# Kernel optimization log

Hardware: AMD Instinct MI355X
Metric: run time of the kernel (lower is better)

Reference implementation:

```python
import jax, jax.numpy as jnp
from jax import lax
import numpy as np

KSIZE = 3  # dynamic depthwise kernel size
DN = ('NCHW', 'OIHW', 'NCHW')


def setup_inputs() -> dict:
    key = jax.random.key(0)
    ks = jax.random.split(key, 6)
    B, C, H, W = 16, 64, 192, 192
    x = jax.random.normal(ks[0], (B, C, H, W), dtype=jnp.float32)
    k_v = jax.random.normal(ks[1], (B, 64), dtype=jnp.float32)
    # kernel-generating MLP (torch nn.Linear weights, y = x @ W.T), scaled for stability
    W1 = jax.random.normal(ks[2], (64, 64), dtype=jnp.float32) * (1.0 / np.sqrt(64))
    W2 = jax.random.normal(ks[3], (C * KSIZE * KSIZE, 64), dtype=jnp.float32) * (1.0 / np.sqrt(64))
    # static Conv2d(C, C, 3, padding=1)
    conv_w = jax.random.normal(ks[4], (C, C, 3, 3), dtype=jnp.float32) * (1.0 / np.sqrt(C * 9))
    conv_b = jax.random.normal(ks[5], (C,), dtype=jnp.float32) * 0.01
    return {"x": x, "k_v": k_v, "W1": W1, "W2": W2, "conv_w": conv_w, "conv_b": conv_b}


def reference(x, k_v, W1, W2, conv_w, conv_b):
    b, c, h, w = x.shape
    pad = (KSIZE - 1) // 2
    # kernel = Linear -> LeakyReLU(0.1) -> Linear, viewed as (b*c, 1, k, k)
    hid = jax.nn.leaky_relu(k_v @ W1.T, negative_slope=0.1)            # (b, 64)
    kern = (hid @ W2.T).reshape(b * c, 1, KSIZE, KSIZE)                # (b*c, 1, k, k)
    # grouped depthwise conv: one distinct kxk kernel per (batch, channel)
    out = lax.conv_general_dilated(
        x.reshape(1, b * c, h, w), kern,
        window_strides=(1, 1), padding=[(pad, pad), (pad, pad)],
        feature_group_count=b * c, dimension_numbers=DN)
    out = jax.nn.leaky_relu(out, negative_slope=0.1).reshape(b, c, h, w)
    # static 3x3 conv residual branch
    res = lax.conv_general_dilated(
        x, conv_w, window_strides=(1, 1), padding=[(1, 1), (1, 1)],
        dimension_numbers=DN) + conv_b[None, :, None, None]
    return out + res
```

## Files before the change

kernel.cpp:

```cpp
#include <hip/hip_runtime.h>

#define B_ 16
#define C_ 64
#define H_ 192
#define W_ 192
#define TR 4
#define TC 64

typedef short bf16x8 __attribute__((ext_vector_type(8)));
typedef float f32x4  __attribute__((ext_vector_type(4)));

static __device__ __forceinline__ unsigned short f2bf(float f) {
    union { float f; unsigned u; } v; v.f = f;
    unsigned r = v.u + 0x7fff + ((v.u >> 16) & 1);
    return (unsigned short)(r >> 16);
}
static __device__ __forceinline__ float bf2f(unsigned short u) {
    union { unsigned u; float f; } v; v.u = ((unsigned)u) << 16; return v.f;
}
static __device__ __forceinline__ int xsw(int p, int ch) {
    return p * 64 + (((ch >> 3) ^ (p & 7)) << 3) + (ch & 7);
}

__global__ void prep(const float* __restrict__ k_v, const float* __restrict__ W1,
                     const float* __restrict__ W2, const float* __restrict__ conv_w,
                     float* __restrict__ kern, unsigned short* __restrict__ wT) {
    const int blk = blockIdx.x, tid = threadIdx.x;
    if (blk < 16) {
        __shared__ float kv[64], hid[64];
        const int b = blk;
        if (tid < 64) kv[tid] = k_v[b * 64 + tid];
        __syncthreads();
        if (tid < 64) {
            const float4* w4 = (const float4*)(W1 + tid * 64);
            float s = 0.f;
#pragma unroll
            for (int k4 = 0; k4 < 16; ++k4) {
                float4 f = w4[k4];
                s += kv[k4 * 4 + 0] * f.x + kv[k4 * 4 + 1] * f.y
                   + kv[k4 * 4 + 2] * f.z + kv[k4 * 4 + 3] * f.w;
            }
            hid[tid] = s > 0.f ? s : 0.1f * s;
        }
        __syncthreads();
        for (int o = tid; o < 576; o += 256) {
            const float4* w4 = (const float4*)(W2 + o * 64);
            float t = 0.f;
#pragma unroll
            for (int k4 = 0; k4 < 16; ++k4) {
                float4 f = w4[k4];
                t += hid[k4 * 4 + 0] * f.x + hid[k4 * 4 + 1] * f.y
                   + hid[k4 * 4 + 2] * f.z + hid[k4 * 4 + 3] * f.w;
            }
            kern[b * 576 + o] = t;
        }
    } else {
        int idx = (blk - 16) * 256 + tid;
        int tap = idx >> 12;
        int rem = idx & 4095;
        int n = rem >> 6, k = rem & 63;
        wT[idx] = f2bf(conv_w[(n * 64 + k) * 9 + tap]);
    }
}

__global__ __launch_bounds__(256)
void fused_conv(const float* __restrict__ x, const unsigned short* __restrict__ wT,
                const float* __restrict__ kern, const float* __restrict__ conv_b,
                float* __restrict__ out) {
    const int L = blockIdx.x + 3 * (blockIdx.y + 48 * blockIdx.z);
    const int g = L & 7;
    const int s = L >> 3;
    const int bx = s % 3;
    const int sl = s / 3;
    const int by = sl % 48;
    const int b  = (g << 1) + (sl / 48);

    const int tid  = threadIdx.x;
    const int lane = tid & 63;
    const int wv   = tid >> 6;
    const int n0   = lane & 15;
    const int q    = lane >> 4;
    const int r0 = by * TR;
    const int c0 = bx * TC;

    __shared__ __align__(16) unsigned short xs[6 * 66 * 64];

    const unsigned short* wbase = wT + n0 * 64 + q * 8;

    for (int u = tid; u < 768; u += 256) {
        int chg  = u / 96;
        int rest = u - chg * 96;
        int row  = rest >> 4;
        int cg   = rest & 15;
        int gr   = r0 + row - 1;
        bool in  = (gr >= 0 && gr < H_);
        int grc  = in ? gr : 0;
        const float* xp = x + ((size_t)(b * 64 + chg * 8) * H_ + grc) * W_ + c0 + cg * 4;
        float4 f[8];
#pragma unroll
        for (int j = 0; j < 8; ++j)
            f[j] = in ? *(const float4*)(xp + j * H_ * W_) : make_float4(0.f, 0.f, 0.f, 0.f);
#pragma unroll
        for (int e = 0; e < 4; ++e) {
            int p = row * 66 + 1 + cg * 4 + e;
            union { bf16x8 v; unsigned short s8[8]; } pk;
#pragma unroll
            for (int j = 0; j < 8; ++j) pk.s8[j] = f2bf(((const float*)&f[j])[e]);
            *(bf16x8*)(xs + xsw(p, chg * 8)) = pk.v;
        }
    }
    if (tid < 96) {
        int chg  = tid / 12;
        int rest = tid - chg * 12;
        int row  = rest >> 1;
        int sc   = (rest & 1) ? 65 : 0;
        int gr = r0 + row - 1, gc = c0 + sc - 1;
        bool in = (gr >= 0 && gr < H_ && gc >= 0 && gc < W_);
        union { bf16x8 v; unsigned short s8[8]; } pk;
#pragma unroll
        for (int j = 0; j < 8; ++j) {
            float vv = 0.f;
            if (in) vv = x[((size_t)(b * 64 + chg * 8 + j) * H_ + gr) * W_ + gc];
            pk.s8[j] = f2bf(vv);
        }
        *(bf16x8*)(xs + xsw(row * 66 + sc, chg * 8)) = pk.v;
    }

    f32x4 acc[4][4];
#pragma unroll
    for (int i = 0; i < 4; ++i)
#pragma unroll
        for (int j = 0; j < 4; ++j) acc[i][j] = (f32x4){0.f, 0.f, 0.f, 0.f};

    __syncthreads();

    int dr = 0, dc = 0;
#pragma unroll 1
    for (int tap = 0; tap < 9; ++tap) {
        bf16x8 bcur[4][2];
#pragma unroll
        for (int nt = 0; nt < 4; ++nt)
#pragma unroll
            for (int ks = 0; ks < 2; ++ks)
                bcur[nt][ks] = *(const bf16x8*)(wbase + tap * 4096 + nt * 1024 + ks * 32);
#pragma unroll
        for (int cb = 0; cb < 4; ++cb) {
            const int p = (wv + dr) * 66 + cb * 16 + n0 + dc;
            bf16x8 a0 = *(const bf16x8*)(xs + p * 64 + ((q ^ (p & 7)) << 3));
            bf16x8 a1 = *(const bf16x8*)(xs + p * 64 + (((q + 4) ^ (p & 7)) << 3));
#pragma unroll
            for (int nt = 0; nt < 4; ++nt) {
                acc[cb][nt] = __builtin_amdgcn_mfma_f32_16x16x32_bf16(a0, bcur[nt][0], acc[cb][nt], 0, 0, 0);
                acc[cb][nt] = __builtin_amdgcn_mfma_f32_16x16x32_bf16(a1, bcur[nt][1], acc[cb][nt], 0, 0, 0);
            }
        }
        if (++dc == 3) { dc = 0; ++dr; }
    }

    const float* kp = kern + b * 576;
#pragma unroll
    for (int nt = 0; nt < 4; ++nt) {
        const int n = nt * 16 + n0;
        float kw[9];
#pragma unroll
        for (int j = 0; j < 9; ++j) kw[j] = kp[n * 9 + j];
        const float bias = conv_b[n];
        const int gn = n >> 3, n7 = n & 7;
#pragma unroll
        for (int cb = 0; cb < 4; ++cb) {
            const int colb = cb * 16 + q * 4;
            float xw[3][6];
#pragma unroll
            for (int d = 0; d < 3; ++d)
#pragma unroll
                for (int cc = 0; cc < 6; ++cc) {
                    int p = (wv + d) * 66 + colb + cc;
                    xw[d][cc] = bf2f(xs[p * 64 + ((gn ^ (p & 7)) << 3) + n7]);
                }
            float4 st;
#pragma unroll
            for (int r = 0; r < 4; ++r) {
                float dw = 0.f;
#pragma unroll
                for (int d = 0; d < 3; ++d)
#pragma unroll
                    for (int e = 0; e < 3; ++e)
                        dw += kw[d * 3 + e] * xw[d][r + e];
                float v = (dw > 0.f ? dw : 0.1f * dw) + acc[cb][nt][r] + bias;
                ((float*)&st)[r] = v;
            }
            *(float4*)(out + ((size_t)(b * 64 + n) * H_ + (r0 + wv)) * W_ + c0 + colb) = st;
        }
    }
}

extern "C" void kernel_launch(void* const* d_in, const int* in_sizes, int n_in,
                              void* d_out, int out_size, void* d_ws, size_t ws_size,
                              hipStream_t stream) {
    const float* x      = (const float*)d_in[0];
    const float* k_v    = (const float*)d_in[1];
    const float* W1     = (const float*)d_in[2];
    const float* W2     = (const float*)d_in[3];
    const float* conv_w = (const float*)d_in[4];
    const float* conv_b = (const float*)d_in[5];
    float* outp = (float*)d_out;

    float* kern        = (float*)d_ws;
    unsigned short* wT = (unsigned short*)((char*)d_ws + 40960);

    prep<<<160, 256, 0, stream>>>(k_v, W1, W2, conv_w, kern, wT);
    dim3 grid(3, 48, 16);
    fused_conv<<<grid, 256, 0, stream>>>(x, wT, kern, conv_b, outp);
}
```

Baseline: 396.3 us.

## Halve row tile and split column blocks across waves to cut registers

Reduces the output tile from 4 rows to 2, so each wave now handles one row and half the column blocks, which halves the accumulator count. The grid doubles and shared memory per block shrinks, aiming for higher occupancy. B-fragment loads move inside the inner loop instead of being held across the tap. The cost is more halo reloading: 4 input rows are staged per 2 output rows instead of 6 per 4.

Result: slower. 415.2 us (+4.8%).

```diff
diff --git a/kernel.cpp b/kernel.cpp
--- a/kernel.cpp
+++ b/kernel.cpp
@@ -4,7 +4,7 @@
 #define C_ 64
 #define H_ 192
 #define W_ 192
-#define TR 4
+#define TR 2
 #define TC 64
 
 typedef short bf16x8 __attribute__((ext_vector_type(8)));
@@ -67,32 +67,34 @@
 void fused_conv(const float* __restrict__ x, const unsigned short* __restrict__ wT,
                 const float* __restrict__ kern, const float* __restrict__ conv_b,
                 float* __restrict__ out) {
-    const int L = blockIdx.x + 3 * (blockIdx.y + 48 * blockIdx.z);
+    const int L = blockIdx.x + 3 * (blockIdx.y + 96 * blockIdx.z);
     const int g = L & 7;
     const int s = L >> 3;
     const int bx = s % 3;
     const int sl = s / 3;
-    const int by = sl % 48;
-    const int b  = (g << 1) + (sl / 48);
+    const int by = sl % 96;
+    const int b  = (g << 1) + (sl / 96);
 
     const int tid  = threadIdx.x;
     const int lane = tid & 63;
     const int wv   = tid >> 6;
     const int n0   = lane & 15;
     const int q    = lane >> 4;
-    const int r0 = by * TR;
-    const int c0 = bx * TC;
-
-    __shared__ __align__(16) unsigned short xs[6 * 66 * 64];
+    const int r0  = by * TR;
+    const int c0  = bx * TC;
+    const int row = wv >> 1;
+    const int cbb = (wv & 1) * 2;
+
+    __shared__ __align__(16) unsigned short xs[4 * 66 * 64];
 
     const unsigned short* wbase = wT + n0 * 64 + q * 8;
 
-    for (int u = tid; u < 768; u += 256) {
-        int chg  = u / 96;
-        int rest = u - chg * 96;
-        int row  = rest >> 4;
+    for (int u = tid; u < 512; u += 256) {
+        int chg  = u >> 6;
+        int rest = u & 63;
+        int rw   = rest >> 4;
         int cg   = rest & 15;
-        int gr   = r0 + row - 1;
+        int gr   = r0 + rw - 1;
         bool in  = (gr >= 0 && gr < H_);
         int grc  = in ? gr : 0;
         const float* xp = x + ((size_t)(b * 64 + chg * 8) * H_ + grc) * W_ + c0 + cg * 4;
@@ -102,19 +104,19 @@
             f[j] = in ? *(const float4*)(xp + j * H_ * W_) : make_float4(0.f, 0.f, 0.f, 0.f);
 #pragma unroll
         for (int e = 0; e < 4; ++e) {
-            int p = row * 66 + 1 + cg * 4 + e;
+            int p = rw * 66 + 1 + cg * 4 + e;
             union { bf16x8 v; unsigned short s8[8]; } pk;
 #pragma unroll
             for (int j = 0; j < 8; ++j) pk.s8[j] = f2bf(((const float*)&f[j])[e]);
             *(bf16x8*)(xs + xsw(p, chg * 8)) = pk.v;
         }
     }
-    if (tid < 96) {
-        int chg  = tid / 12;
-        int rest = tid - chg * 12;
-        int row  = rest >> 1;
+    if (tid < 64) {
+        int chg  = tid >> 3;
+        int rest = tid & 7;
+        int rw   = rest >> 1;
         int sc   = (rest & 1) ? 65 : 0;
-        int gr = r0 + row - 1, gc = c0 + sc - 1;
+        int gr = r0 + rw - 1, gc = c0 + sc - 1;
         bool in = (gr >= 0 && gr < H_ && gc >= 0 && gc < W_);
         union { bf16x8 v; unsigned short s8[8]; } pk;
 #pragma unroll
@@ -123,12 +125,12 @@
             if (in) vv = x[((size_t)(b * 64 + chg * 8 + j) * H_ + gr) * W_ + gc];
             pk.s8[j] = f2bf(vv);
         }
-        *(bf16x8*)(xs + xsw(row * 66 + sc, chg * 8)) = pk.v;
-    }
-
-    f32x4 acc[4][4];
-#pragma unroll
-    for (int i = 0; i < 4; ++i)
+        *(bf16x8*)(xs + xsw(rw * 66 + sc, chg * 8)) = pk.v;
+    }
+
+    f32x4 acc[2][4];
+#pragma unroll
+    for (int i = 0; i < 2; ++i)
 #pragma unroll
         for (int j = 0; j < 4; ++j) acc[i][j] = (f32x4){0.f, 0.f, 0.f, 0.f};
 
@@ -137,21 +139,17 @@
     int dr = 0, dc = 0;
 #pragma unroll 1
     for (int tap = 0; tap < 9; ++tap) {
-        bf16x8 bcur[4][2];
-#pragma unroll
-        for (int nt = 0; nt < 4; ++nt)
-#pragma unroll
-            for (int ks = 0; ks < 2; ++ks)
-                bcur[nt][ks] = *(const bf16x8*)(wbase + tap * 4096 + nt * 1024 + ks * 32);
-#pragma unroll
-        for (int cb = 0; cb < 4; ++cb) {
-            const int p = (wv + dr) * 66 + cb * 16 + n0 + dc;
+#pragma unroll
+        for (int cbi = 0; cbi < 2; ++cbi) {
+            const int p = (row + dr) * 66 + (cbb + cbi) * 16 + n0 + dc;
             bf16x8 a0 = *(const bf16x8*)(xs + p * 64 + ((q ^ (p & 7)) << 3));
             bf16x8 a1 = *(const bf16x8*)(xs + p * 64 + (((q + 4) ^ (p & 7)) << 3));
 #pragma unroll
             for (int nt = 0; nt < 4; ++nt) {
-                acc[cb][nt] = __builtin_amdgcn_mfma_f32_16x16x32_bf16(a0, bcur[nt][0], acc[cb][nt], 0, 0, 0);
-                acc[cb][nt] = __builtin_amdgcn_mfma_f32_16x16x32_bf16(a1, bcur[nt][1], acc[cb][nt], 0, 0, 0);
+                bf16x8 b0 = *(const bf16x8*)(wbase + tap * 4096 + nt * 1024);
+                bf16x8 b1 = *(const bf16x8*)(wbase + tap * 4096 + nt * 1024 + 32);
+                acc[cbi][nt] = __builtin_amdgcn_mfma_f32_16x16x32_bf16(a0, b0, acc[cbi][nt], 0, 0, 0);
+                acc[cbi][nt] = __builtin_amdgcn_mfma_f32_16x16x32_bf16(a1, b1, acc[cbi][nt], 0, 0, 0);
             }
         }
         if (++dc == 3) { dc = 0; ++dr; }
@@ -167,14 +165,14 @@
         const float bias = conv_b[n];
         const int gn = n >> 3, n7 = n & 7;
 #pragma unroll
-        for (int cb = 0; cb < 4; ++cb) {
-            const int colb = cb * 16 + q * 4;
+        for (int cbi = 0; cbi < 2; ++cbi) {
+            const int colb = (cbb + cbi) * 16 + q * 4;
             float xw[3][6];
 #pragma unroll
             for (int d = 0; d < 3; ++d)
 #pragma unroll
                 for (int cc = 0; cc < 6; ++cc) {
-                    int p = (wv + d) * 66 + colb + cc;
+                    int p = (row + d) * 66 + colb + cc;
                     xw[d][cc] = bf2f(xs[p * 64 + ((gn ^ (p & 7)) << 3) + n7]);
                 }
             float4 st;
@@ -186,10 +184,10 @@
 #pragma unroll
                     for (int e = 0; e < 3; ++e)
                         dw += kw[d * 3 + e] * xw[d][r + e];
-                float v = (dw > 0.f ? dw : 0.1f * dw) + acc[cb][nt][r] + bias;
+                float v = (dw > 0.f ? dw : 0.1f * dw) + acc[cbi][nt][r] + bias;
                 ((float*)&st)[r] = v;
             }
-            *(float4*)(out + ((size_t)(b * 64 + n) * H_ + (r0 + wv)) * W_ + c0 + colb) = st;
+            *(float4*)(out + ((size_t)(b * 64 + n) * H_ + (r0 + row)) * W_ + c0 + colb) = st;
         }
     }
 }
@@ -209,6 +207,6 @@
     unsigned short* wT = (unsigned short*)((char*)d_ws + 40960);
 
     prep<<<160, 256, 0, stream>>>(k_v, W1, W2, conv_w, kern, wT);
-    dim3 grid(3, 48, 16);
+    dim3 grid(3, 96, 16);
     fused_conv<<<grid, 256, 0, stream>>>(x, wT, kern, conv_b, outp);
 }
```
